# Optimization experiments

Measured on AMD Instinct MI355X. Metric: run time of the kernel, lower is better.

Reference implementation:

```python
import jax, jax.numpy as jnp
import numpy as np

MARGIN = 1.0

def _pairwise_sqdist(z):
    # ||zi - zj||^2 = ||zi||^2 + ||zj||^2 - 2 zi.zj
    sq = jnp.sum(z * z, axis=-1)  # [N]
    d2 = sq[:, None] + sq[None, :] - 2.0 * (z @ z.T)
    return jnp.maximum(d2, 0.0)

def _safe_sqrt(d2):
    # sqrt with well-defined gradient at 0 (matches cdist values; diag = 0)
    pos = d2 > 0.0
    return jnp.where(pos, jnp.sqrt(jnp.where(pos, d2, 1.0)), 0.0)

def setup_inputs() -> dict:
    key = jax.random.key(0)
    k1, k2 = jax.random.split(key)
    z = jax.random.normal(k1, (8192, 128), dtype=jnp.float32)
    labels = jax.random.randint(k2, (8192,), 0, 100, dtype=jnp.int64)
    return {"z": z, "labels": labels}

def reference(z, labels):
    d2 = _pairwise_sqdist(z)              # [N, N] squared distances
    dist = _safe_sqrt(d2)                 # [N, N] distances
    label_eq = labels[:, None] == labels[None, :]
    pos = jnp.where(label_eq, d2, 0.0)
    neg = jnp.where(label_eq, 0.0, jnp.square(jax.nn.relu(MARGIN - dist)))
    return jnp.mean(pos + neg)
```

## Files before the change

kernel.cpp:

```cpp
#include <hip/hip_runtime.h>
#include <stdint.h>


#define NROWS 8192
#define DIMK  128
#define NB    64
#define NPAIR (NB * (NB + 1) / 2)
#define NBLK  (NPAIR * 2)

typedef __attribute__((ext_vector_type(4))) float f32x4;

#define AS_GLOBAL __attribute__((address_space(1)))
#define AS_LDS    __attribute__((address_space(3)))

__global__ __launch_bounds__(256) void prep_kernel(
    const float* __restrict__ z, unsigned char* __restrict__ zb,
    float* __restrict__ sq) {
  int tid = threadIdx.x;
  int row = (blockIdx.x << 3) + (tid >> 5);
  int c32 = tid & 31;
  float4 x = ((const float4*)(z + (size_t)row * DIMK))[c32];
  int u = __builtin_amdgcn_cvt_pk_fp8_f32(x.x, x.y, 0, false);
  u     = __builtin_amdgcn_cvt_pk_fp8_f32(x.z, x.w, u, true);
  float r0 = __builtin_amdgcn_cvt_f32_fp8(u, 0);
  float r1 = __builtin_amdgcn_cvt_f32_fp8(u, 1);
  float r2 = __builtin_amdgcn_cvt_f32_fp8(u, 2);
  float r3 = __builtin_amdgcn_cvt_f32_fp8(u, 3);
  float s = (r0 * r0 + r1 * r1) + (r2 * r2 + r3 * r3);
  int k0 = c32 << 2;
  int g  = (((k0 >> 3) & 3) << 2) | (k0 >> 5);
  int p  = ((g ^ (row & 15)) << 3) + (k0 & 7);
  *(uint32_t*)(zb + (size_t)row * DIMK + p) = (uint32_t)u;
  #pragma unroll
  for (int off = 16; off; off >>= 1) s += __shfl_down(s, off, 32);
  if (c32 == 0) sq[row] = s;
}

__global__ __launch_bounds__(256, 6) void loss_kernel(
    const unsigned char* __restrict__ zb, const float* __restrict__ sq,
    const int* __restrict__ labels, float* __restrict__ partials) {
  __shared__ __align__(16) unsigned char ldsA[8192];
  __shared__ __align__(16) unsigned char ldsB[16384];
  __shared__ __align__(16) float sqAl[64];
  __shared__ __align__(16) float sqBl[128];
  __shared__ __align__(16) int   laAl[64];
  __shared__ __align__(16) int   laBl[128];
  __shared__ float red[4];

  int tid = threadIdx.x, lane = tid & 63, wave = tid >> 6;

  int bid = blockIdx.x;
  int t = bid >> 1, h = bid & 1;
  #define TRI(rr) ((rr) * NB - ((rr) * ((rr) - 1)) / 2)
  int r = (int)(((float)(2 * NB + 1) -
                 sqrtf((float)((2 * NB + 1) * (2 * NB + 1) - 8 * t))) * 0.5f);
  if (r < 0) r = 0; if (r > NB - 1) r = NB - 1;
  while (TRI(r + 1) <= t) ++r;
  while (TRI(r) > t) --r;
  int bi = r, bj = t - TRI(r) + r;
  int row0 = (bi << 7) + (h << 6);
  int col0 = (bj << 7);

  const unsigned char* Ab = zb + (size_t)row0 * DIMK;
  const unsigned char* Bb = zb + (size_t)col0 * DIMK;
  #pragma unroll
  for (int it = 0; it < 2; ++it) {
    int L0 = (it << 8) + (wave << 6);
    __builtin_amdgcn_global_load_lds(
        (const AS_GLOBAL void*)(uintptr_t)(Ab + (size_t)(L0 + lane) * 16),
        (AS_LDS void*)(uintptr_t)(ldsA + (size_t)L0 * 16), 16, 0, 0);
  }
  #pragma unroll
  for (int it = 0; it < 4; ++it) {
    int L0 = (it << 8) + (wave << 6);
    __builtin_amdgcn_global_load_lds(
        (const AS_GLOBAL void*)(uintptr_t)(Bb + (size_t)(L0 + lane) * 16),
        (AS_LDS void*)(uintptr_t)(ldsB + (size_t)L0 * 16), 16, 0, 0);
  }
  if (tid < 64) {
    sqAl[tid] = sq[row0 + tid];
    laAl[tid] = labels[row0 + tid];
  } else if (tid < 192) {
    int t2 = tid - 64;
    sqBl[t2] = sq[col0 + t2];
    laBl[t2] = labels[col0 + t2];
  }
  asm volatile("s_waitcnt vmcnt(0)" ::: "memory");
  __syncthreads();

  int wm = wave >> 1, wn = wave & 1;
  int lc = lane & 15;
  int q  = lane >> 4;
  f32x4 acc[2][4] = {};
  #pragma unroll
  for (int ks = 0; ks < 4; ++ks) {
    int so = ((((q << 2) | ks) ^ lc) << 3);
    long a0 = *(const long*)(ldsA + ((wm << 5)      + lc) * 128 + so);
    long a1 = *(const long*)(ldsA + ((wm << 5) + 16 + lc) * 128 + so);
    long b0 = *(const long*)(ldsB + ((wn << 6)      + lc) * 128 + so);
    long b1 = *(const long*)(ldsB + ((wn << 6) + 16 + lc) * 128 + so);
    long b2 = *(const long*)(ldsB + ((wn << 6) + 32 + lc) * 128 + so);
    long b3 = *(const long*)(ldsB + ((wn << 6) + 48 + lc) * 128 + so);
    acc[0][0] = __builtin_amdgcn_mfma_f32_16x16x32_fp8_fp8(a0, b0, acc[0][0], 0, 0, 0);
    acc[0][1] = __builtin_amdgcn_mfma_f32_16x16x32_fp8_fp8(a0, b1, acc[0][1], 0, 0, 0);
    acc[0][2] = __builtin_amdgcn_mfma_f32_16x16x32_fp8_fp8(a0, b2, acc[0][2], 0, 0, 0);
    acc[0][3] = __builtin_amdgcn_mfma_f32_16x16x32_fp8_fp8(a0, b3, acc[0][3], 0, 0, 0);
    acc[1][0] = __builtin_amdgcn_mfma_f32_16x16x32_fp8_fp8(a1, b0, acc[1][0], 0, 0, 0);
    acc[1][1] = __builtin_amdgcn_mfma_f32_16x16x32_fp8_fp8(a1, b1, acc[1][1], 0, 0, 0);
    acc[1][2] = __builtin_amdgcn_mfma_f32_16x16x32_fp8_fp8(a1, b2, acc[1][2], 0, 0, 0);
    acc[1][3] = __builtin_amdgcn_mfma_f32_16x16x32_fp8_fp8(a1, b3, acc[1][3], 0, 0, 0);
  }

  int r0 = q << 2;
  float sn_[4]; int ln_[4];
  #pragma unroll
  for (int j = 0; j < 4; ++j) {
    int n = (wn << 6) + (j << 4) + lc;
    sn_[j] = sqBl[n]; ln_[j] = laBl[n];
  }
  float ps0 = 0.f, ps1 = 0.f, ps2 = 0.f, ps3 = 0.f;
  float mnall = 1e30f;
  #pragma unroll
  for (int i = 0; i < 2; ++i) {
    int mb = (wm << 5) + (i << 4) + r0;
    f32x4 sm4 = *(const f32x4*)&sqAl[mb];
    int4  lm4 = *(const int4*)&laAl[mb];
    #pragma unroll
    for (int j = 0; j < 4; ++j) {
      float d0  = fmaf(-2.f, acc[i][j][0], sm4[0] + sn_[j]);
      float d1  = fmaf(-2.f, acc[i][j][1], sm4[1] + sn_[j]);
      float d2_ = fmaf(-2.f, acc[i][j][2], sm4[2] + sn_[j]);
      float d3  = fmaf(-2.f, acc[i][j][3], sm4[3] + sn_[j]);
      mnall = fminf(mnall, fminf(fminf(d0, d1), fminf(d2_, d3)));
      ps0 += (lm4.x == ln_[j]) ? d0  : 0.f;
      ps1 += (lm4.y == ln_[j]) ? d1  : 0.f;
      ps2 += (lm4.z == ln_[j]) ? d2_ : 0.f;
      ps3 += (lm4.w == ln_[j]) ? d3  : 0.f;
    }
  }
  if (__builtin_expect(__any(mnall < 1.f), 0)) {
    ps0 = ps1 = ps2 = ps3 = 0.f;
    #pragma unroll
    for (int i = 0; i < 2; ++i) {
      int mb = (wm << 5) + (i << 4) + r0;
      f32x4 sm4 = *(const f32x4*)&sqAl[mb];
      int4  lm4 = *(const int4*)&laAl[mb];
      #pragma unroll
      for (int j = 0; j < 4; ++j) {
        float dc, tt;
        dc = fmaxf(fmaf(-2.f, acc[i][j][0], sm4[0] + sn_[j]), 0.f);
        tt = fmaxf(1.f - sqrtf(dc), 0.f);
        ps0 += (lm4.x == ln_[j]) ? dc : tt * tt;
        dc = fmaxf(fmaf(-2.f, acc[i][j][1], sm4[1] + sn_[j]), 0.f);
        tt = fmaxf(1.f - sqrtf(dc), 0.f);
        ps1 += (lm4.y == ln_[j]) ? dc : tt * tt;
        dc = fmaxf(fmaf(-2.f, acc[i][j][2], sm4[2] + sn_[j]), 0.f);
        tt = fmaxf(1.f - sqrtf(dc), 0.f);
        ps2 += (lm4.z == ln_[j]) ? dc : tt * tt;
        dc = fmaxf(fmaf(-2.f, acc[i][j][3], sm4[3] + sn_[j]), 0.f);
        tt = fmaxf(1.f - sqrtf(dc), 0.f);
        ps3 += (lm4.w == ln_[j]) ? dc : tt * tt;
      }
    }
  }
  float psum = (ps0 + ps1) + (ps2 + ps3);
  float w = (bi == bj) ? 1.f : 2.f;
  psum *= w * (1.f / (8192.f * 8192.f));

  #pragma unroll
  for (int off = 32; off; off >>= 1) psum += __shfl_down(psum, off);
  if (lane == 0) red[wave] = psum;
  __syncthreads();
  if (tid == 0)
    partials[bid] = (red[0] + red[1]) + (red[2] + red[3]);
}

__global__ __launch_bounds__(256) void reduce_kernel(
    const float* __restrict__ partials, float* __restrict__ out) {
  int tid = threadIdx.x, lane = tid & 63, wave = tid >> 6;
  float s = 0.f;
  for (int k = tid; k < NBLK; k += 256) s += partials[k];
  #pragma unroll
  for (int off = 32; off; off >>= 1) s += __shfl_down(s, off);
  __shared__ float red[4];
  if (lane == 0) red[wave] = s;
  __syncthreads();
  if (tid == 0) out[0] = red[0] + red[1] + red[2] + red[3];
}

extern "C" void kernel_launch(void* const* d_in, const int* in_sizes, int n_in,
                              void* d_out, int out_size, void* d_ws, size_t ws_size,
                              hipStream_t stream) {
  const float* z      = (const float*)d_in[0];
  const int*   labels = (const int*)d_in[1];
  float*       out    = (float*)d_out;
  unsigned char* zb   = (unsigned char*)d_ws;
  char* p = (char*)d_ws + (size_t)NROWS * DIMK;
  float* sq       = (float*)p;
  float* partials = (float*)(p + NROWS * 4);

  prep_kernel<<<NROWS / 8, 256, 0, stream>>>(z, zb, sq);
  loss_kernel<<<NBLK, 256, 0, stream>>>(zb, sq, labels, partials);
  reduce_kernel<<<1, 256, 0, stream>>>(partials, out);
}
```

Before: 78.02 us.

## Make loss kernel persistent with double-buffered LDS tile prefetch

Replaces the one-block-per-half-tile grid with 512 persistent 512-thread blocks. Each block walks the triangular tile list with a stride of 512 and prefetches the next 128x128 tile's fp8 rows, squared norms and labels into a second LDS buffer, overlapping that load with the current tile's MFMA and epilogue. The aim is to hide global-to-LDS latency and cut block launch and partial-write overhead. In exchange LDS use per block grows to about 68 KB, which limits occupancy, and the 2080 tiles split unevenly across 512 blocks, so some blocks do one more tile than others.

Result: faster. 73.03 us (-6.4%).

```diff
diff --git a/kernel.cpp b/kernel.cpp
--- a/kernel.cpp
+++ b/kernel.cpp
@@ -5,8 +5,8 @@
 #define NROWS 8192
 #define DIMK  128
 #define NB    64
-#define NPAIR (NB * (NB + 1) / 2)
-#define NBLK  (NPAIR * 2)
+#define NTILE (NB * (NB + 1) / 2)
+#define NPERS 512
 
 typedef __attribute__((ext_vector_type(4))) float f32x4;
 
@@ -36,110 +36,129 @@
   if (c32 == 0) sq[row] = s;
 }
 
-__global__ __launch_bounds__(256, 6) void loss_kernel(
-    const unsigned char* __restrict__ zb, const float* __restrict__ sq,
-    const int* __restrict__ labels, float* __restrict__ partials) {
-  __shared__ __align__(16) unsigned char ldsA[8192];
-  __shared__ __align__(16) unsigned char ldsB[16384];
-  __shared__ __align__(16) float sqAl[64];
-  __shared__ __align__(16) float sqBl[128];
-  __shared__ __align__(16) int   laAl[64];
-  __shared__ __align__(16) int   laBl[128];
-  __shared__ float red[4];
-
-  int tid = threadIdx.x, lane = tid & 63, wave = tid >> 6;
-
-  int bid = blockIdx.x;
-  int t = bid >> 1, h = bid & 1;
+__device__ __forceinline__ void decode_tile(int t, int& bi, int& bj) {
   #define TRI(rr) ((rr) * NB - ((rr) * ((rr) - 1)) / 2)
   int r = (int)(((float)(2 * NB + 1) -
                  sqrtf((float)((2 * NB + 1) * (2 * NB + 1) - 8 * t))) * 0.5f);
   if (r < 0) r = 0; if (r > NB - 1) r = NB - 1;
   while (TRI(r + 1) <= t) ++r;
   while (TRI(r) > t) --r;
-  int bi = r, bj = t - TRI(r) + r;
-  int row0 = (bi << 7) + (h << 6);
-  int col0 = (bj << 7);
-
-  const unsigned char* Ab = zb + (size_t)row0 * DIMK;
-  const unsigned char* Bb = zb + (size_t)col0 * DIMK;
-  #pragma unroll
-  for (int it = 0; it < 2; ++it) {
-    int L0 = (it << 8) + (wave << 6);
-    __builtin_amdgcn_global_load_lds(
-        (const AS_GLOBAL void*)(uintptr_t)(Ab + (size_t)(L0 + lane) * 16),
-        (AS_LDS void*)(uintptr_t)(ldsA + (size_t)L0 * 16), 16, 0, 0);
-  }
-  #pragma unroll
-  for (int it = 0; it < 4; ++it) {
-    int L0 = (it << 8) + (wave << 6);
-    __builtin_amdgcn_global_load_lds(
-        (const AS_GLOBAL void*)(uintptr_t)(Bb + (size_t)(L0 + lane) * 16),
-        (AS_LDS void*)(uintptr_t)(ldsB + (size_t)L0 * 16), 16, 0, 0);
-  }
-  if (tid < 64) {
-    sqAl[tid] = sq[row0 + tid];
-    laAl[tid] = labels[row0 + tid];
-  } else if (tid < 192) {
-    int t2 = tid - 64;
-    sqBl[t2] = sq[col0 + t2];
-    laBl[t2] = labels[col0 + t2];
-  }
-  asm volatile("s_waitcnt vmcnt(0)" ::: "memory");
-  __syncthreads();
-
+  bi = r; bj = t - TRI(r) + r;
+}
+
+__global__ __launch_bounds__(512, 4) void loss_kernel(
+    const unsigned char* __restrict__ zb, const float* __restrict__ sq,
+    const int* __restrict__ labels, float* __restrict__ partials) {
+  __shared__ __align__(16) unsigned char buf[2][32768];
+  __shared__ __align__(16) unsigned char sqlab[2][2048];
+  __shared__ float red[8];
+
+  int tid = threadIdx.x, lane = tid & 63, wave = tid >> 6;
   int wm = wave >> 1, wn = wave & 1;
   int lc = lane & 15;
   int q  = lane >> 4;
-  f32x4 acc[2][4] = {};
-  #pragma unroll
-  for (int ks = 0; ks < 4; ++ks) {
-    int so = ((((q << 2) | ks) ^ lc) << 3);
-    long a0 = *(const long*)(ldsA + ((wm << 5)      + lc) * 128 + so);
-    long a1 = *(const long*)(ldsA + ((wm << 5) + 16 + lc) * 128 + so);
-    long b0 = *(const long*)(ldsB + ((wn << 6)      + lc) * 128 + so);
-    long b1 = *(const long*)(ldsB + ((wn << 6) + 16 + lc) * 128 + so);
-    long b2 = *(const long*)(ldsB + ((wn << 6) + 32 + lc) * 128 + so);
-    long b3 = *(const long*)(ldsB + ((wn << 6) + 48 + lc) * 128 + so);
-    acc[0][0] = __builtin_amdgcn_mfma_f32_16x16x32_fp8_fp8(a0, b0, acc[0][0], 0, 0, 0);
-    acc[0][1] = __builtin_amdgcn_mfma_f32_16x16x32_fp8_fp8(a0, b1, acc[0][1], 0, 0, 0);
-    acc[0][2] = __builtin_amdgcn_mfma_f32_16x16x32_fp8_fp8(a0, b2, acc[0][2], 0, 0, 0);
-    acc[0][3] = __builtin_amdgcn_mfma_f32_16x16x32_fp8_fp8(a0, b3, acc[0][3], 0, 0, 0);
-    acc[1][0] = __builtin_amdgcn_mfma_f32_16x16x32_fp8_fp8(a1, b0, acc[1][0], 0, 0, 0);
-    acc[1][1] = __builtin_amdgcn_mfma_f32_16x16x32_fp8_fp8(a1, b1, acc[1][1], 0, 0, 0);
-    acc[1][2] = __builtin_amdgcn_mfma_f32_16x16x32_fp8_fp8(a1, b2, acc[1][2], 0, 0, 0);
-    acc[1][3] = __builtin_amdgcn_mfma_f32_16x16x32_fp8_fp8(a1, b3, acc[1][3], 0, 0, 0);
+
+  int sl_isB  = wave >> 2;
+  int sl_isLa = (wave >> 1) & 1;
+  int sl_half = wave & 1;
+
+  float psum_acc = 0.f;
+
+  int b = blockIdx.x;
+  int bi, bj;
+  decode_tile(b, bi, bj);
+
+  {
+    const unsigned char* Ab = zb + (((size_t)bi << 7) * DIMK);
+    const unsigned char* Bb = zb + (((size_t)bj << 7) * DIMK);
+    #pragma unroll
+    for (int it = 0; it < 2; ++it) {
+      int L0 = (it << 9) + (wave << 6);
+      __builtin_amdgcn_global_load_lds(
+          (const AS_GLOBAL void*)(uintptr_t)(Ab + (size_t)(L0 + lane) * 16),
+          (AS_LDS void*)(uintptr_t)(&buf[0][(size_t)L0 * 16]), 16, 0, 0);
+      __builtin_amdgcn_global_load_lds(
+          (const AS_GLOBAL void*)(uintptr_t)(Bb + (size_t)(L0 + lane) * 16),
+          (AS_LDS void*)(uintptr_t)(&buf[0][16384 + (size_t)L0 * 16]), 16, 0, 0);
+    }
+    const char* p0 = sl_isLa ? (const char*)labels : (const char*)sq;
+    const char* src = p0 + ((size_t)((sl_isB ? bj : bi) << 7) << 2)
+                         + (sl_half << 8);
+    if (lane < 16)
+      __builtin_amdgcn_global_load_lds(
+          (const AS_GLOBAL void*)(uintptr_t)(src + lane * 16),
+          (AS_LDS void*)(uintptr_t)(&sqlab[0][wave << 8]), 16, 0, 0);
   }
 
-  int r0 = q << 2;
-  float sn_[4]; int ln_[4];
-  #pragma unroll
-  for (int j = 0; j < 4; ++j) {
-    int n = (wn << 6) + (j << 4) + lc;
-    sn_[j] = sqBl[n]; ln_[j] = laBl[n];
-  }
-  float ps0 = 0.f, ps1 = 0.f, ps2 = 0.f, ps3 = 0.f;
-  float mnall = 1e30f;
-  #pragma unroll
-  for (int i = 0; i < 2; ++i) {
-    int mb = (wm << 5) + (i << 4) + r0;
-    f32x4 sm4 = *(const f32x4*)&sqAl[mb];
-    int4  lm4 = *(const int4*)&laAl[mb];
+  int cur = 0;
+  for (int t = b; ; t += NPERS) {
+    int tn = t + NPERS;
+    bool hasNext = tn < NTILE;
+
+    asm volatile("s_waitcnt vmcnt(0)" ::: "memory");
+    __syncthreads();
+
+    int bin = bi, bjn = bj;
+    if (hasNext) {
+      decode_tile(tn, bin, bjn);
+      int nc = cur ^ 1;
+      const unsigned char* Ab = zb + (((size_t)bin << 7) * DIMK);
+      const unsigned char* Bb = zb + (((size_t)bjn << 7) * DIMK);
+      #pragma unroll
+      for (int it = 0; it < 2; ++it) {
+        int L0 = (it << 9) + (wave << 6);
+        __builtin_amdgcn_global_load_lds(
+            (const AS_GLOBAL void*)(uintptr_t)(Ab + (size_t)(L0 + lane) * 16),
+            (AS_LDS void*)(uintptr_t)(&buf[nc][(size_t)L0 * 16]), 16, 0, 0);
+        __builtin_amdgcn_global_load_lds(
+            (const AS_GLOBAL void*)(uintptr_t)(Bb + (size_t)(L0 + lane) * 16),
+            (AS_LDS void*)(uintptr_t)(&buf[nc][16384 + (size_t)L0 * 16]), 16, 0, 0);
+      }
+      const char* p0 = sl_isLa ? (const char*)labels : (const char*)sq;
+      const char* src = p0 + ((size_t)((sl_isB ? bjn : bin) << 7) << 2)
+                           + (sl_half << 8);
+      if (lane < 16)
+        __builtin_amdgcn_global_load_lds(
+            (const AS_GLOBAL void*)(uintptr_t)(src + lane * 16),
+            (AS_LDS void*)(uintptr_t)(&sqlab[nc][wave << 8]), 16, 0, 0);
+    }
+
+    const unsigned char* ldsA = &buf[cur][0];
+    const unsigned char* ldsB = &buf[cur][16384];
+    const float* sqAl = (const float*)&sqlab[cur][0];
+    const int*   laAl = (const int*)&sqlab[cur][512];
+    const float* sqBl = (const float*)&sqlab[cur][1024];
+    const int*   laBl = (const int*)&sqlab[cur][1536];
+
+    f32x4 acc[2][4] = {};
+    #pragma unroll
+    for (int ks = 0; ks < 4; ++ks) {
+      int so = ((((q << 2) | ks) ^ lc) << 3);
+      long a0 = *(const long*)(ldsA + ((wm << 5)      + lc) * 128 + so);
+      long a1 = *(const long*)(ldsA + ((wm << 5) + 16 + lc) * 128 + so);
+      long b0 = *(const long*)(ldsB + ((wn << 6)      + lc) * 128 + so);
+      long b1 = *(const long*)(ldsB + ((wn << 6) + 16 + lc) * 128 + so);
+      long b2 = *(const long*)(ldsB + ((wn << 6) + 32 + lc) * 128 + so);
+      long b3 = *(const long*)(ldsB + ((wn << 6) + 48 + lc) * 128 + so);
+      acc[0][0] = __builtin_amdgcn_mfma_f32_16x16x32_fp8_fp8(a0, b0, acc[0][0], 0, 0, 0);
+      acc[0][1] = __builtin_amdgcn_mfma_f32_16x16x32_fp8_fp8(a0, b1, acc[0][1], 0, 0, 0);
+      acc[0][2] = __builtin_amdgcn_mfma_f32_16x16x32_fp8_fp8(a0, b2, acc[0][2], 0, 0, 0);
+      acc[0][3] = __builtin_amdgcn_mfma_f32_16x16x32_fp8_fp8(a0, b3, acc[0][3], 0, 0, 0);
+      acc[1][0] = __builtin_amdgcn_mfma_f32_16x16x32_fp8_fp8(a1, b0, acc[1][0], 0, 0, 0);
+      acc[1][1] = __builtin_amdgcn_mfma_f32_16x16x32_fp8_fp8(a1, b1, acc[1][1], 0, 0, 0);
+      acc[1][2] = __builtin_amdgcn_mfma_f32_16x16x32_fp8_fp8(a1, b2, acc[1][2], 0, 0, 0);
+      acc[1][3] = __builtin_amdgcn_mfma_f32_16x16x32_fp8_fp8(a1, b3, acc[1][3], 0, 0, 0);
+    }
+
+    int r0 = q << 2;
+    float sn_[4]; int ln_[4];
     #pragma unroll
     for (int j = 0; j < 4; ++j) {
-      float d0  = fmaf(-2.f, acc[i][j][0], sm4[0] + sn_[j]);
-      float d1  = fmaf(-2.f, acc[i][j][1], sm4[1] + sn_[j]);
-      float d2_ = fmaf(-2.f, acc[i][j][2], sm4[2] + sn_[j]);
-      float d3  = fmaf(-2.f, acc[i][j][3], sm4[3] + sn_[j]);
-      mnall = fminf(mnall, fminf(fminf(d0, d1), fminf(d2_, d3)));
-      ps0 += (lm4.x == ln_[j]) ? d0  : 0.f;
-      ps1 += (lm4.y == ln_[j]) ? d1  : 0.f;
-      ps2 += (lm4.z == ln_[j]) ? d2_ : 0.f;
-      ps3 += (lm4.w == ln_[j]) ? d3  : 0.f;
-    }
-  }
-  if (__builtin_expect(__any(mnall < 1.f), 0)) {
-    ps0 = ps1 = ps2 = ps3 = 0.f;
+      int n = (wn << 6) + (j << 4) + lc;
+      sn_[j] = sqBl[n]; ln_[j] = laBl[n];
+    }
+    float ps0 = 0.f, ps1 = 0.f, ps2 = 0.f, ps3 = 0.f;
+    float mnall = 1e30f;
     #pragma unroll
     for (int i = 0; i < 2; ++i) {
       int mb = (wm << 5) + (i << 4) + r0;
@@ -147,39 +166,67 @@
       int4  lm4 = *(const int4*)&laAl[mb];
       #pragma unroll
       for (int j = 0; j < 4; ++j) {
-        float dc, tt;
-        dc = fmaxf(fmaf(-2.f, acc[i][j][0], sm4[0] + sn_[j]), 0.f);
-        tt = fmaxf(1.f - sqrtf(dc), 0.f);
-        ps0 += (lm4.x == ln_[j]) ? dc : tt * tt;
-        dc = fmaxf(fmaf(-2.f, acc[i][j][1], sm4[1] + sn_[j]), 0.f);
-        tt = fmaxf(1.f - sqrtf(dc), 0.f);
-        ps1 += (lm4.y == ln_[j]) ? dc : tt * tt;
-        dc = fmaxf(fmaf(-2.f, acc[i][j][2], sm4[2] + sn_[j]), 0.f);
-        tt = fmaxf(1.f - sqrtf(dc), 0.f);
-        ps2 += (lm4.z == ln_[j]) ? dc : tt * tt;
-        dc = fmaxf(fmaf(-2.f, acc[i][j][3], sm4[3] + sn_[j]), 0.f);
-        tt = fmaxf(1.f - sqrtf(dc), 0.f);
-        ps3 += (lm4.w == ln_[j]) ? dc : tt * tt;
+        float d0  = fmaf(-2.f, acc[i][j][0], sm4[0] + sn_[j]);
+        float d1  = fmaf(-2.f, acc[i][j][1], sm4[1] + sn_[j]);
+        float d2_ = fmaf(-2.f, acc[i][j][2], sm4[2] + sn_[j]);
+        float d3  = fmaf(-2.f, acc[i][j][3], sm4[3] + sn_[j]);
+        mnall = fminf(mnall, fminf(fminf(d0, d1), fminf(d2_, d3)));
+        ps0 += (lm4.x == ln_[j]) ? d0  : 0.f;
+        ps1 += (lm4.y == ln_[j]) ? d1  : 0.f;
+        ps2 += (lm4.z == ln_[j]) ? d2_ : 0.f;
+        ps3 += (lm4.w == ln_[j]) ? d3  : 0.f;
       }
     }
+    if (__builtin_expect(__any(mnall < 1.f), 0)) {
+      ps0 = ps1 = ps2 = ps3 = 0.f;
+      #pragma unroll
+      for (int i = 0; i < 2; ++i) {
+        int mb = (wm << 5) + (i << 4) + r0;
+        f32x4 sm4 = *(const f32x4*)&sqAl[mb];
+        int4  lm4 = *(const int4*)&laAl[mb];
+        #pragma unroll
+        for (int j = 0; j < 4; ++j) {
+          float dc, tt;
+          dc = fmaxf(fmaf(-2.f, acc[i][j][0], sm4[0] + sn_[j]), 0.f);
+          tt = fmaxf(1.f - sqrtf(dc), 0.f);
+          ps0 += (lm4.x == ln_[j]) ? dc : tt * tt;
+          dc = fmaxf(fmaf(-2.f, acc[i][j][1], sm4[1] + sn_[j]), 0.f);
+          tt = fmaxf(1.f - sqrtf(dc), 0.f);
+          ps1 += (lm4.y == ln_[j]) ? dc : tt * tt;
+          dc = fmaxf(fmaf(-2.f, acc[i][j][2], sm4[2] + sn_[j]), 0.f);
+          tt = fmaxf(1.f - sqrtf(dc), 0.f);
+          ps2 += (lm4.z == ln_[j]) ? dc : tt * tt;
+          dc = fmaxf(fmaf(-2.f, acc[i][j][3], sm4[3] + sn_[j]), 0.f);
+          tt = fmaxf(1.f - sqrtf(dc), 0.f);
+          ps3 += (lm4.w == ln_[j]) ? dc : tt * tt;
+        }
+      }
+    }
+    float w = (bi == bj) ? 1.f : 2.f;
+    psum_acc += w * ((ps0 + ps1) + (ps2 + ps3));
+
+    if (!hasNext) break;
+    bi = bin; bj = bjn; cur ^= 1;
   }
-  float psum = (ps0 + ps1) + (ps2 + ps3);
-  float w = (bi == bj) ? 1.f : 2.f;
-  psum *= w * (1.f / (8192.f * 8192.f));
-
+
+  psum_acc *= (1.f / (8192.f * 8192.f));
   #pragma unroll
-  for (int off = 32; off; off >>= 1) psum += __shfl_down(psum, off);
-  if (lane == 0) red[wave] = psum;
+  for (int off = 32; off; off >>= 1) psum_acc += __shfl_down(psum_acc, off);
+  if (lane == 0) red[wave] = psum_acc;
   __syncthreads();
-  if (tid == 0)
-    partials[bid] = (red[0] + red[1]) + (red[2] + red[3]);
+  if (tid == 0) {
+    float s = 0.f;
+    #pragma unroll
+    for (int k = 0; k < 8; ++k) s += red[k];
+    partials[blockIdx.x] = s;
+  }
 }
 
 __global__ __launch_bounds__(256) void reduce_kernel(
     const float* __restrict__ partials, float* __restrict__ out) {
   int tid = threadIdx.x, lane = tid & 63, wave = tid >> 6;
   float s = 0.f;
-  for (int k = tid; k < NBLK; k += 256) s += partials[k];
+  for (int k = tid; k < NPERS; k += 256) s += partials[k];
   #pragma unroll
   for (int off = 32; off; off >>= 1) s += __shfl_down(s, off);
   __shared__ float red[4];
@@ -200,6 +247,6 @@
   float* partials = (float*)(p + NROWS * 4);
 
   prep_kernel<<<NROWS / 8, 256, 0, stream>>>(z, zb, sq);
-  loss_kernel<<<NBLK, 256, 0, stream>>>(zb, sq, labels, partials);
+  loss_kernel<<<NPERS, 512, 0, stream>>>(zb, sq, labels, partials);
   reduce_kernel<<<1, 256, 0, stream>>>(partials, out);
 }
```
